# Performance work log

Hardware: AMD Instinct MI355X
Metric: run time of the kernel (lower is better)

## Reference

```python
import jax, jax.numpy as jnp
import numpy as np

B, N, DIM, H = 8, 4096, 768, 12
HD = DIM // H
SCALE = HD ** -0.5


def setup_inputs() -> dict:
    key = jax.random.key(0)
    ks = jax.random.split(key, 6)
    x = jax.random.normal(ks[0], (B, N, DIM), dtype=jnp.float32)
    # torch nn.Linear weights: [out_features, in_features]
    Wqkv = jax.random.normal(ks[1], (3 * DIM, DIM), dtype=jnp.float32) * (DIM ** -0.5)
    Wp = jax.random.normal(ks[2], (DIM, DIM), dtype=jnp.float32) * (DIM ** -0.5)
    bp = jnp.zeros((DIM,), dtype=jnp.float32)
    w_q = jax.random.normal(ks[3], (H, HD), dtype=jnp.float32)
    w_k = jax.random.normal(ks[4], (H, HD), dtype=jnp.float32)
    return {"x": x, "Wqkv": Wqkv, "Wp": Wp, "bp": bp, "w_q": w_q, "w_k": w_k}


def reference(x, Wqkv, Wp, bp, w_q, w_k):
    b, n, c = x.shape
    qkv = x @ Wqkv.T                                   # [B,N,3C]
    # rearrange 'B N (qkv H C) -> qkv B H N C'
    qkv = qkv.reshape(b, n, 3, H, HD).transpose(2, 0, 3, 1, 4)
    q, k, v = qkv[0], qkv[1], qkv[2]                   # each [B,H,N,hd]

    alpha = jnp.einsum('bhnc,hc->bhn', q, w_q) * SCALE
    alpha = jax.nn.softmax(alpha, axis=-1)             # [B,H,N]
    global_q = jnp.einsum('bhn,bhnc->bhc', alpha, q)   # [B,H,hd]

    p = global_q[:, :, None, :] * k                    # [B,H,N,hd]
    beta = jnp.einsum('bhnc,hc->bhn', p, w_k) * SCALE
    beta = jax.nn.softmax(beta, axis=-1)
    global_k = jnp.einsum('bhn,bhnc->bhc', beta, k)    # [B,H,hd]

    u = global_k[:, :, None, :] * v                    # [B,H,N,hd]
    q_flat = q.transpose(0, 2, 1, 3).reshape(b, n, c)  # 'B H N C -> B N (H C)'
    u_flat = u.transpose(0, 2, 1, 3).reshape(b, n, c)
    return u_flat @ Wp.T + bp + q_flat
```

## Files before the change

kernel.cpp:

```cpp
#include <hip/hip_runtime.h>
#include <hip/hip_bf16.h>
#include <cstdint>
#include <cstddef>

#define B_ 8
#define N_ 4096
#define DIM_ 768
#define H_ 12
#define M_ (B_*N_)
#define SCALE_ 0.125f
#define NS2 16
#define KDIM 768
#define NKT 12
#define NITER 6
#define QKS 1536

typedef __attribute__((ext_vector_type(8))) short s8v;
typedef __attribute__((ext_vector_type(4))) float f4v;

__device__ inline float bf2f(unsigned short u) {
    unsigned v = ((unsigned)u) << 16;
    return __builtin_bit_cast(float, v);
}
__device__ inline unsigned short f2bf(float f) {
    unsigned u = __builtin_bit_cast(unsigned, f);
    return (unsigned short)((u + 0x7FFFu + ((u >> 16) & 1u)) >> 16);
}
__device__ inline void gload16(const void* g, void* l) {
    __builtin_amdgcn_global_load_lds(
        (const __attribute__((address_space(1))) void*)g,
        (__attribute__((address_space(3))) void*)l, 16, 0, 0);
}

#define BARX() __builtin_amdgcn_s_barrier()
#define PRIO1() __builtin_amdgcn_s_setprio(1)
#define PRIO0() __builtin_amdgcn_s_setprio(0)
#define VM4() asm volatile("s_waitcnt vmcnt(4)" ::: "memory")
#define VM0() asm volatile("s_waitcnt vmcnt(0)" ::: "memory")

template<int EPI>
__global__ __launch_bounds__(512, 2)
void gemm8(const unsigned short* __restrict__ A, int ldaE,
           const unsigned short* __restrict__ Bmat,
           unsigned short* __restrict__ Cb,
           const float* __restrict__ w_q,
           float* __restrict__ pv1, float* __restrict__ pms1,
           int Nc, int ntn)
{
    __shared__ __align__(16) char smem[131072];
    const int tid = threadIdx.x;
    const int l = tid & 63, w = tid >> 6;
    const int lr = l & 15, g = l >> 4;
    const int wm = w >> 2, wn = w & 3;

    const int nwg = gridDim.x, cpx = nwg >> 3;
    const int bid = blockIdx.x;
    int lg = (bid & 7) * cpx + (bid >> 3);

    size_t batch_off = 0;
    if (EPI == 2) {
        const int bb = lg / 9;
        lg -= bb * 9;
        batch_off = (size_t)bb * (DIM_ * DIM_);
    }
    const int tm = lg / ntn, tn = lg % ntn;
    const int m0 = tm * 256, n0 = tn * 256;

    const long ldaB = (long)ldaE * 2;
    const long ldbB = (long)KDIM * 2;

    const int srA = w * 8 + (l >> 3);
    const int kbs = (l & 7) * 16;
    const int kbx = kbs ^ ((srA & 7) << 4);
    long offA[2], offB[2];
    offA[0] = (long)(srA) * ldaB + kbx;
    offA[1] = (long)(128 + srA) * ldaB + kbx;
    offB[0] = (long)(((srA >> 5)) * 64 + (srA & 31)) * ldbB + kbx;
    offB[1] = (long)((2 + (srA >> 5)) * 64 + (srA & 31)) * ldbB + kbx;

    const char* Abase = (const char*)(A + batch_off + (size_t)m0 * ldaE);
    const char* Bbase = (const char*)(Bmat + (size_t)n0 * KDIM);

    const int aoff = (wm * 64 + lr) * 128;
    const int boff = (wn * 32 + lr) * 128;
    const int kx0 = (g * 16) ^ ((lr & 7) << 4);
    const int kx1 = (64 + g * 16) ^ ((lr & 7) << 4);

    f4v acc[8][4] = {};
    s8v af[4][2];
    s8v bfr[2][2][2];

#define STG_A(buf_, qm_, kt_) { \
    const char* s0_ = Abase + (long)(kt_) * 2 + (long)(qm_) * 64 * ldaB; \
    char* d0_ = smem + ((buf_) * 4 + (qm_)) * 16384 + w * 1024; \
    gload16(s0_ + offA[0], d0_); \
    gload16(s0_ + offA[1], d0_ + 8192); }

#define STG_B(buf_, qn_, kt_) { \
    const char* s0_ = Bbase + (long)(kt_) * 2 + (long)(qn_) * 32 * ldbB; \
    char* d0_ = smem + ((buf_) * 4 + 2 + (qn_)) * 16384 + w * 1024; \
    gload16(s0_ + offB[0], d0_); \
    gload16(s0_ + offB[1], d0_ + 8192); }

#define DS_A(buf_, qm_) { \
    const char* ba_ = smem + ((buf_) * 4 + (qm_)) * 16384 + aoff; \
    af[0][0] = *(const s8v*)(ba_ +    0 + kx0); af[0][1] = *(const s8v*)(ba_ +    0 + kx1); \
    af[1][0] = *(const s8v*)(ba_ + 2048 + kx0); af[1][1] = *(const s8v*)(ba_ + 2048 + kx1); \
    af[2][0] = *(const s8v*)(ba_ + 4096 + kx0); af[2][1] = *(const s8v*)(ba_ + 4096 + kx1); \
    af[3][0] = *(const s8v*)(ba_ + 6144 + kx0); af[3][1] = *(const s8v*)(ba_ + 6144 + kx1); }

#define DS_B(buf_, qn_) { \
    const char* bb_ = smem + ((buf_) * 4 + 2 + (qn_)) * 16384 + boff; \
    bfr[qn_][0][0] = *(const s8v*)(bb_ +    0 + kx0); bfr[qn_][0][1] = *(const s8v*)(bb_ +    0 + kx1); \
    bfr[qn_][1][0] = *(const s8v*)(bb_ + 2048 + kx0); bfr[qn_][1][1] = *(const s8v*)(bb_ + 2048 + kx1); }

#define MM(fmg_, fng_, qn_, kk_) \
    acc[fmg_][fng_] = __builtin_amdgcn_mfma_f32_16x16x32_bf16(af[(fmg_)&3][kk_], bfr[qn_][(fng_)&1][kk_], acc[fmg_][fng_], 0, 0, 0);

#define MFMA8(qm_, qn_, kk_) \
    MM((qm_)*4+0, (qn_)*2+0, qn_, kk_) MM((qm_)*4+0, (qn_)*2+1, qn_, kk_) \
    MM((qm_)*4+1, (qn_)*2+0, qn_, kk_) MM((qm_)*4+1, (qn_)*2+1, qn_, kk_) \
    MM((qm_)*4+2, (qn_)*2+0, qn_, kk_) MM((qm_)*4+2, (qn_)*2+1, qn_, kk_) \
    MM((qm_)*4+3, (qn_)*2+0, qn_, kk_) MM((qm_)*4+3, (qn_)*2+1, qn_, kk_)

#define MFMA16(qm_, qn_) { MFMA8(qm_, qn_, 0) MFMA8(qm_, qn_, 1) }

    STG_A(0, 0, 0); STG_B(0, 0, 0); STG_A(0, 1, 0); STG_B(0, 1, 0);
    STG_A(1, 0, 64); STG_B(1, 0, 64);
    VM4(); BARX();

    for (int i = 0; i < NITER; ++i) {
        const int t1k = (2 * i + 1) * 64, t2k = (2 * i + 2) * 64, t3k = (2 * i + 3) * 64;
        const bool h2 = (2 * i + 2) < NKT, h3 = (2 * i + 3) < NKT;
        const bool last = (i == NITER - 1);
        DS_A(0, 0); DS_B(0, 0); STG_B(1, 1, t1k);
        BARX(); PRIO1(); MFMA16(0, 0); PRIO0(); BARX();
        DS_B(0, 1); STG_A(1, 1, t1k);
        BARX(); PRIO1(); MFMA16(0, 1); PRIO0(); BARX();
        DS_A(0, 1); if (h2) STG_A(0, 0, t2k);
        BARX(); PRIO1(); MFMA16(1, 0); PRIO0(); BARX();
        if (h2) STG_B(0, 0, t2k);
        BARX(); PRIO1(); MFMA16(1, 1); PRIO0();
        if (last) { VM0(); } else { VM4(); }
        BARX();
        DS_A(1, 0); DS_B(1, 0); if (h2) STG_A(0, 1, t2k);
        BARX(); PRIO1(); MFMA16(0, 0); PRIO0(); BARX();
        DS_B(1, 1); if (h2) STG_B(0, 1, t2k);
        BARX(); PRIO1(); MFMA16(0, 1); PRIO0(); BARX();
        DS_A(1, 1); if (h3) STG_A(1, 0, t3k);
        BARX(); PRIO1(); MFMA16(1, 0); PRIO0(); BARX();
        if (h3) STG_B(1, 0, t3k);
        BARX(); PRIO1(); MFMA16(1, 1); PRIO0();
        if (last) { VM0(); } else { VM4(); }
        BARX();
    }

#pragma unroll
    for (int fmg = 0; fmg < 8; ++fmg) {
#pragma unroll
        for (int fng = 0; fng < 4; ++fng) {
            const int col = n0 + wn * 64 + fng * 16 + lr;
#pragma unroll
            for (int r = 0; r < 4; ++r) {
                const int row = m0 + wm * 128 + fmg * 16 + g * 4 + r;
                Cb[batch_off + (size_t)row * Nc + col] = f2bf(acc[fmg][fng][r]);
            }
        }
    }

    if (EPI == 0 && tn < 3) {
        const int h = tn * 4 + wn;
        float wq[4];
#pragma unroll
        for (int f = 0; f < 4; ++f) wq[f] = w_q[h * 64 + f * 16 + lr];

        float d[8][4];
#pragma unroll
        for (int fmg = 0; fmg < 8; ++fmg) {
#pragma unroll
            for (int r = 0; r < 4; ++r) {
                float s = acc[fmg][0][r] * wq[0] + acc[fmg][1][r] * wq[1]
                        + acc[fmg][2][r] * wq[2] + acc[fmg][3][r] * wq[3];
                s += __shfl_xor(s, 1); s += __shfl_xor(s, 2);
                s += __shfl_xor(s, 4); s += __shfl_xor(s, 8);
                d[fmg][r] = s * SCALE_;
            }
        }
        float mw = d[0][0];
#pragma unroll
        for (int fmg = 0; fmg < 8; ++fmg)
#pragma unroll
            for (int r = 0; r < 4; ++r) mw = fmaxf(mw, d[fmg][r]);
        mw = fmaxf(mw, __shfl_xor(mw, 16));
        mw = fmaxf(mw, __shfl_xor(mw, 32));

        float ssum = 0.f;
        float pvec[4] = {};
#pragma unroll
        for (int fmg = 0; fmg < 8; ++fmg) {
#pragma unroll
            for (int r = 0; r < 4; ++r) {
                const float e = __expf(d[fmg][r] - mw);
                ssum += e;
#pragma unroll
                for (int f = 0; f < 4; ++f) pvec[f] += e * acc[fmg][f][r];
            }
        }
        ssum += __shfl_xor(ssum, 16); ssum += __shfl_xor(ssum, 32);
#pragma unroll
        for (int f = 0; f < 4; ++f) {
            pvec[f] += __shfl_xor(pvec[f], 16);
            pvec[f] += __shfl_xor(pvec[f], 32);
        }

        const int b = m0 >> 12;
        const int bh = b * H_ + h;
        const int slice = ((m0 & (N_ - 1)) >> 7) + wm;
        if (g == 0) {
#pragma unroll
            for (int f = 0; f < 4; ++f)
                pv1[(size_t)(bh * 32 + slice) * 64 + f * 16 + lr] = pvec[f];
            if (lr == 0) {
                pms1[(bh * 32 + slice) * 2] = mw;
                pms1[(bh * 32 + slice) * 2 + 1] = ssum;
            }
        }
    }
#undef STG_A
#undef STG_B
#undef DS_A
#undef DS_B
#undef MM
#undef MFMA8
#undef MFMA16
}

__global__ __launch_bounds__(512, 2)
void gemm128(const unsigned short* __restrict__ A, int ldaE,
             const unsigned short* __restrict__ Bmat,
             float* __restrict__ Cf,
             const float* __restrict__ bias, const unsigned short* __restrict__ Qf,
             int Nc, int ntn)
{
    __shared__ __align__(16) char smem[98304];
    const int tid = threadIdx.x;
    const int l = tid & 63, w = tid >> 6;
    const int lr = l & 15, g = l >> 4;
    const int wm = w >> 2, wn = w & 3;

    const int nwg = gridDim.x, cpx = nwg >> 3;
    const int bid = blockIdx.x;
    const int lg = (bid & 7) * cpx + (bid >> 3);
    const int tm = lg / ntn, tn = lg % ntn;
    const int m0 = tm * 128, n0 = tn * 256;

    const long ldaB = (long)ldaE * 2;
    const long ldbB = (long)KDIM * 2;

    const unsigned short* Bp = Bmat + (size_t)(m0 >> 12) * (DIM_ * DIM_);

    const int srA = w * 8 + (l >> 3);
    const int kbs = (l & 7) * 16;
    const int kbx = kbs ^ ((srA & 7) << 4);
    long offA[2], offB[2];
    offA[0] = (long)(srA) * ldaB + kbx;
    offA[1] = (long)(64 + srA) * ldaB + kbx;
    offB[0] = (long)(((srA >> 5)) * 64 + (srA & 31)) * ldbB + kbx;
    offB[1] = (long)((2 + (srA >> 5)) * 64 + (srA & 31)) * ldbB + kbx;

    const char* Abase = (const char*)(A + (size_t)m0 * ldaE);
    const char* Bbase = (const char*)(Bp + (size_t)n0 * KDIM);

    const int aoff = (wm * 64 + lr) * 128;
    const int boff = (wn * 32 + lr) * 128;
    const int kx0 = (g * 16) ^ ((lr & 7) << 4);
    const int kx1 = (64 + g * 16) ^ ((lr & 7) << 4);

    f4v acc[4][4] = {};
    s8v af[4][2];
    s8v bfr[2][2][2];

#define STG_A1(buf_, kt_) { \
    const char* s0_ = Abase + (long)(kt_) * 2; \
    char* d0_ = smem + ((buf_) * 3) * 16384 + w * 1024; \
    gload16(s0_ + offA[0], d0_); \
    gload16(s0_ + offA[1], d0_ + 8192); }

#define STG_B1(buf_, qn_, kt_) { \
    const char* s0_ = Bbase + (long)(kt_) * 2 + (long)(qn_) * 32 * ldbB; \
    char* d0_ = smem + ((buf_) * 3 + 1 + (qn_)) * 16384 + w * 1024; \
    gload16(s0_ + offB[0], d0_); \
    gload16(s0_ + offB[1], d0_ + 8192); }

#define DS_A1(buf_) { \
    const char* ba_ = smem + ((buf_) * 3) * 16384 + aoff; \
    af[0][0] = *(const s8v*)(ba_ +    0 + kx0); af[0][1] = *(const s8v*)(ba_ +    0 + kx1); \
    af[1][0] = *(const s8v*)(ba_ + 2048 + kx0); af[1][1] = *(const s8v*)(ba_ + 2048 + kx1); \
    af[2][0] = *(const s8v*)(ba_ + 4096 + kx0); af[2][1] = *(const s8v*)(ba_ + 4096 + kx1); \
    af[3][0] = *(const s8v*)(ba_ + 6144 + kx0); af[3][1] = *(const s8v*)(ba_ + 6144 + kx1); }

#define DS_B1(buf_, qn_) { \
    const char* bb_ = smem + ((buf_) * 3 + 1 + (qn_)) * 16384 + boff; \
    bfr[qn_][0][0] = *(const s8v*)(bb_ +    0 + kx0); bfr[qn_][0][1] = *(const s8v*)(bb_ +    0 + kx1); \
    bfr[qn_][1][0] = *(const s8v*)(bb_ + 2048 + kx0); bfr[qn_][1][1] = *(const s8v*)(bb_ + 2048 + kx1); }

#define MM1(fm_, fng_, qn_, kk_) \
    acc[fm_][fng_] = __builtin_amdgcn_mfma_f32_16x16x32_bf16(af[fm_][kk_], bfr[qn_][(fng_)&1][kk_], acc[fm_][fng_], 0, 0, 0);

#define MFMA16_1(qn_, kk_) \
    MM1(0, (qn_)*2+0, qn_, kk_) MM1(0, (qn_)*2+1, qn_, kk_) \
    MM1(1, (qn_)*2+0, qn_, kk_) MM1(1, (qn_)*2+1, qn_, kk_) \
    MM1(2, (qn_)*2+0, qn_, kk_) MM1(2, (qn_)*2+1, qn_, kk_) \
    MM1(3, (qn_)*2+0, qn_, kk_) MM1(3, (qn_)*2+1, qn_, kk_)

#define MFMA32_1(qn_) { MFMA16_1(qn_, 0) MFMA16_1(qn_, 1) }

    STG_A1(0, 0); STG_B1(0, 0, 0); STG_B1(0, 1, 0);
    STG_A1(1, 64); STG_B1(1, 0, 64);
    VM4(); BARX();

    for (int i = 0; i < NITER; ++i) {
        const int t1k = (2 * i + 1) * 64, t2k = (2 * i + 2) * 64, t3k = (2 * i + 3) * 64;
        const bool h2 = (2 * i + 2) < NKT, h3 = (2 * i + 3) < NKT;
        const bool last = (i == NITER - 1);
        DS_A1(0); DS_B1(0, 0); STG_B1(1, 1, t1k);
        BARX(); PRIO1(); MFMA32_1(0); PRIO0(); BARX();
        DS_B1(0, 1); if (h2) { STG_A1(0, t2k); STG_B1(0, 0, t2k); }
        BARX(); PRIO1(); MFMA32_1(1); PRIO0();
        if (last) { VM0(); } else { VM4(); }
        BARX();
        DS_A1(1); DS_B1(1, 0); if (h2) STG_B1(0, 1, t2k);
        BARX(); PRIO1(); MFMA32_1(0); PRIO0(); BARX();
        DS_B1(1, 1); if (h3) { STG_A1(1, t3k); STG_B1(1, 0, t3k); }
        BARX(); PRIO1(); MFMA32_1(1); PRIO0();
        if (last) { VM0(); } else { VM4(); }
        BARX();
    }

#pragma unroll
    for (int fm = 0; fm < 4; ++fm) {
#pragma unroll
        for (int fng = 0; fng < 4; ++fng) {
            const int col = n0 + wn * 64 + fng * 16 + lr;
#pragma unroll
            for (int r = 0; r < 4; ++r) {
                const int row = m0 + wm * 64 + fm * 16 + g * 4 + r;
                Cf[(size_t)row * Nc + col] = acc[fm][fng][r] + bias[col]
                                             + bf2f(Qf[(size_t)row * QKS + col]);
            }
        }
    }
#undef STG_A1
#undef STG_B1
#undef DS_A1
#undef DS_B1
#undef MM1
#undef MFMA16_1
#undef MFMA32_1
}

__global__ __launch_bounds__(256)
void fused_path(const unsigned short* __restrict__ qkv, int col_off,
                const float* __restrict__ vec, int per_bh,
                float* __restrict__ partv, float* __restrict__ partms)
{
    const int bid = blockIdx.x;
    const int bh = bid / NS2, sp = bid % NS2;
    const int b = bh / H_, h = bh % H_;
    const int t = threadIdx.x;
    const int lane8 = t & 7, grp = t >> 3;

    const unsigned short* base = qkv + ((size_t)(b * N_ + sp * 256) * QKS)
                                 + col_off + h * 64 + lane8 * 8;
    const float* wv = vec + (per_bh ? bh * 64 : h * 64) + lane8 * 8;
    float w8[8];
#pragma unroll
    for (int j = 0; j < 8; j++) w8[j] = wv[j];

    float q[8][8];
    float d[8];
#pragma unroll
    for (int pass = 0; pass < 8; ++pass) {
        const int row = pass * 32 + grp;
        s8v q8 = *(const s8v*)(base + (size_t)row * QKS);
        float s = 0.f;
#pragma unroll
        for (int j = 0; j < 8; j++) {
            q[pass][j] = bf2f((unsigned short)q8[j]);
            s += q[pass][j] * w8[j];
        }
        s += __shfl_xor(s, 1); s += __shfl_xor(s, 2); s += __shfl_xor(s, 4);
        d[pass] = s * SCALE_;
    }
    float m = d[0];
#pragma unroll
    for (int pass = 1; pass < 8; ++pass) m = fmaxf(m, d[pass]);
    float ssum = 0.f;
    float a8[8] = {};
#pragma unroll
    for (int pass = 0; pass < 8; ++pass) {
        float e = __expf(d[pass] - m);
        ssum += e;
#pragma unroll
        for (int j = 0; j < 8; j++) a8[j] += e * q[pass][j];
    }

    __shared__ float Lm[32], Ls[32];
    __shared__ float La[32][64];
    if (lane8 == 0) { Lm[grp] = m; Ls[grp] = ssum; }
#pragma unroll
    for (int j = 0; j < 8; j++) La[grp][lane8 * 8 + j] = a8[j];
    __syncthreads();

    if (t < 64) {
        float mstar = Lm[0];
#pragma unroll
        for (int g2 = 1; g2 < 32; ++g2) mstar = fmaxf(mstar, Lm[g2]);
        float sstar = 0.f, v = 0.f;
#pragma unroll
        for (int g2 = 0; g2 < 32; ++g2) {
            float e = __expf(Lm[g2] - mstar);
            sstar += Ls[g2] * e;
            v += La[g2][t] * e;
        }
        partv[(size_t)bid * 64 + t] = v;
        if (t == 0) { partms[bid * 2] = mstar; partms[bid * 2 + 1] = sstar; }
    }
}

__global__ void path_reduce(const float* __restrict__ partv, const float* __restrict__ partms,
                            int nsp, float* __restrict__ gout,
                            const float* __restrict__ wk, float* __restrict__ bvec)
{
    const int bh = blockIdx.x;
    const int t = threadIdx.x;
    const int h = bh % H_;
    float mstar = partms[(bh * nsp) * 2];
    for (int p = 1; p < nsp; ++p) mstar = fmaxf(mstar, partms[(bh * nsp + p) * 2]);
    float sstar = 0.f, v = 0.f;
    for (int p = 0; p < nsp; ++p) {
        float e = __expf(partms[(bh * nsp + p) * 2] - mstar);
        sstar += partms[(bh * nsp + p) * 2 + 1] * e;
        v += partv[(size_t)(bh * nsp + p) * 64 + t] * e;
    }
    float g = v / sstar;
    gout[bh * 64 + t] = g;
    if (wk) bvec[bh * 64 + t] = g * wk[h * 64 + t];
}

__global__ void cvt_all(const float* __restrict__ x, const float* __restrict__ Wqkv,
                        unsigned short* __restrict__ xb, unsigned short* __restrict__ wqkb,
                        unsigned short* __restrict__ wvT,
                        int n4x, int n4xw)
{
    int i = blockIdx.x * 256 + threadIdx.x;
    if (i < n4xw) {
        const float* src; unsigned short* dst; int k;
        if (i < n4x) { src = x; dst = xb; k = i; }
        else { src = Wqkv; dst = wqkb; k = i - n4x; }
        float4 v = ((const float4*)src)[k];
        ushort4 o;
        o.x = f2bf(v.x); o.y = f2bf(v.y); o.z = f2bf(v.z); o.w = f2bf(v.w);
        ((ushort4*)dst)[k] = o;
    } else {
        const int k = i - n4xw;
        const int ii = k % DIM_;
        const int c0 = (k / DIM_) * 4;
        ushort4 o;
        o.x = f2bf(Wqkv[(size_t)(2 * DIM_ + c0 + 0) * DIM_ + ii]);
        o.y = f2bf(Wqkv[(size_t)(2 * DIM_ + c0 + 1) * DIM_ + ii]);
        o.z = f2bf(Wqkv[(size_t)(2 * DIM_ + c0 + 2) * DIM_ + ii]);
        o.w = f2bf(Wqkv[(size_t)(2 * DIM_ + c0 + 3) * DIM_ + ii]);
        *(ushort4*)&wvT[(size_t)ii * DIM_ + c0] = o;
    }
}

__global__ __launch_bounds__(256)
void fold_wp(const float* __restrict__ Wp, const float* __restrict__ gk,
             unsigned short* __restrict__ W2)
{
    int idx = blockIdx.x * 256 + threadIdx.x;
    int e4 = idx * 4;
    int b = (int)((unsigned)e4 / (unsigned)(DIM_ * DIM_));
    int rem = e4 - b * (DIM_ * DIM_);
    int c = rem % DIM_;
    float4 wv = *(const float4*)&Wp[rem];
    const float* gp = &gk[b * DIM_ + c];
    ushort4 o;
    o.x = f2bf(wv.x * gp[0]); o.y = f2bf(wv.y * gp[1]);
    o.z = f2bf(wv.z * gp[2]); o.w = f2bf(wv.w * gp[3]);
    *(ushort4*)&W2[e4] = o;
}

extern "C" void kernel_launch(void* const* d_in, const int* in_sizes, int n_in,
                              void* d_out, int out_size, void* d_ws, size_t ws_size,
                              hipStream_t stream)
{
    const float* x    = (const float*)d_in[0];
    const float* Wqkv = (const float*)d_in[1];
    const float* Wp   = (const float*)d_in[2];
    const float* bp   = (const float*)d_in[3];
    const float* w_q  = (const float*)d_in[4];
    const float* w_k  = (const float*)d_in[5];
    float* out = (float*)d_out;

    constexpr size_t NXB  = (size_t)M_ * DIM_;
    constexpr size_t NWQK = (size_t)2 * DIM_ * DIM_;
    constexpr size_t NWV  = (size_t)DIM_ * DIM_;
    constexpr size_t NQK  = (size_t)M_ * QKS;
    constexpr size_t NW2  = (size_t)B_ * DIM_ * DIM_;

    char* p = (char*)d_ws;
    unsigned short* xb    = (unsigned short*)p; p += NXB * 2;
    unsigned short* wqkb  = (unsigned short*)p; p += NWQK * 2;
    unsigned short* wvT   = (unsigned short*)p; p += NWV * 2;
    unsigned short* qkb   = (unsigned short*)p; p += NQK * 2;
    unsigned short* w2b   = (unsigned short*)p; p += NW2 * 2;
    unsigned short* w3b   = (unsigned short*)p; p += NW2 * 2;
    float* pv1  = (float*)p; p += (size_t)B_ * H_ * 32 * 64 * 4;
    float* pms1 = (float*)p; p += (size_t)B_ * H_ * 32 * 2 * 4;
    float* pv2  = (float*)p; p += (size_t)B_ * H_ * NS2 * 64 * 4;
    float* pms2 = (float*)p; p += (size_t)B_ * H_ * NS2 * 2 * 4;
    float* gq   = (float*)p; p += (size_t)B_ * H_ * 64 * 4;
    float* bvec = (float*)p; p += (size_t)B_ * H_ * 64 * 4;
    float* gkv  = (float*)p; p += (size_t)B_ * H_ * 64 * 4;

    constexpr int N4X  = (int)(NXB / 4);
    constexpr int N4XW = N4X + (int)(NWQK / 4);
    constexpr int NTOT = N4XW + (int)(NWV / 4);
    cvt_all<<<NTOT / 256, 256, 0, stream>>>(x, Wqkv, xb, wqkb, wvT, N4X, N4XW);

    gemm8<0><<<128 * 6, 512, 0, stream>>>(xb, DIM_, wqkb, qkb, w_q, pv1, pms1, QKS, 6);

    path_reduce<<<B_ * H_, 64, 0, stream>>>(pv1, pms1, 32, gq, w_k, bvec);

    fused_path<<<B_ * H_ * NS2, 256, 0, stream>>>(qkb, DIM_, bvec, 1, pv2, pms2);
    path_reduce<<<B_ * H_, 64, 0, stream>>>(pv2, pms2, NS2, gkv, nullptr, nullptr);

    fold_wp<<<(int)(NW2 / 4 / 256), 256, 0, stream>>>(Wp, gkv, w2b);

    gemm8<2><<<72, 512, 0, stream>>>(w2b, DIM_, wvT, w3b, nullptr, nullptr, nullptr,
                                     DIM_, 3);

    gemm128<<<256 * 3, 512, 0, stream>>>(xb, DIM_, w3b, out, bp, qkb, DIM_, 3);
}
```

Baseline: 236.9 us.

## Fold q residual into projection weights and fuse first path reduction

The q residual is folded algebraically into the per-batch combined weight: gemm8<2> now adds the fp32 Wq rows to the folded Wp*diag(gk)*Wv product, so the final GEMM no longer reads q from a workspace. Because of this, the QKV GEMM stops storing q entirely and writes only the k columns into a narrower buffer. The first path_reduce is merged into the k-path kernel, and each block recomputes global_q from the partials, which removes one launch. The cost is redundant per-block reduction work and q entering the final GEMM at bf16 precision through the weights, with its rounding behaviour changed.

```diff
diff --git a/kernel.cpp b/kernel.cpp
--- a/kernel.cpp
+++ b/kernel.cpp
@@ -13,7 +13,6 @@
 #define KDIM 768
 #define NKT 12
 #define NITER 6
-#define QKS 1536
 
 typedef __attribute__((ext_vector_type(8))) short s8v;
 typedef __attribute__((ext_vector_type(4))) float f4v;
@@ -45,7 +44,8 @@
            unsigned short* __restrict__ Cb,
            const float* __restrict__ w_q,
            float* __restrict__ pv1, float* __restrict__ pms1,
-           int Nc, int ntn)
+           const float* __restrict__ addW,
+           int ntn)
 {
     __shared__ __align__(16) char smem[131072];
     const int tid = threadIdx.x;
@@ -155,15 +155,34 @@
         BARX();
     }
 
-#pragma unroll
-    for (int fmg = 0; fmg < 8; ++fmg) {
-#pragma unroll
-        for (int fng = 0; fng < 4; ++fng) {
-            const int col = n0 + wn * 64 + fng * 16 + lr;
-#pragma unroll
-            for (int r = 0; r < 4; ++r) {
-                const int row = m0 + wm * 128 + fmg * 16 + g * 4 + r;
-                Cb[batch_off + (size_t)row * Nc + col] = f2bf(acc[fmg][fng][r]);
+    if (EPI == 0) {
+        if (tn >= 3) {
+            const int c0 = (tn - 3) * 256;
+#pragma unroll
+            for (int fmg = 0; fmg < 8; ++fmg) {
+#pragma unroll
+                for (int fng = 0; fng < 4; ++fng) {
+                    const int col = c0 + wn * 64 + fng * 16 + lr;
+#pragma unroll
+                    for (int r = 0; r < 4; ++r) {
+                        const int row = m0 + wm * 128 + fmg * 16 + g * 4 + r;
+                        Cb[(size_t)row * DIM_ + col] = f2bf(acc[fmg][fng][r]);
+                    }
+                }
+            }
+        }
+    } else {
+#pragma unroll
+        for (int fmg = 0; fmg < 8; ++fmg) {
+#pragma unroll
+            for (int fng = 0; fng < 4; ++fng) {
+                const int col = n0 + wn * 64 + fng * 16 + lr;
+#pragma unroll
+                for (int r = 0; r < 4; ++r) {
+                    const int row = m0 + wm * 128 + fmg * 16 + g * 4 + r;
+                    Cb[batch_off + (size_t)row * DIM_ + col] =
+                        f2bf(acc[fmg][fng][r] + addW[(size_t)row * DIM_ + col]);
+                }
             }
         }
     }
@@ -239,7 +258,7 @@
 void gemm128(const unsigned short* __restrict__ A, int ldaE,
              const unsigned short* __restrict__ Bmat,
              float* __restrict__ Cf,
-             const float* __restrict__ bias, const unsigned short* __restrict__ Qf,
+             const float* __restrict__ bias,
              int Nc, int ntn)
 {
     __shared__ __align__(16) char smem[98304];
@@ -345,8 +364,7 @@
 #pragma unroll
             for (int r = 0; r < 4; ++r) {
                 const int row = m0 + wm * 64 + fm * 16 + g * 4 + r;
-                Cf[(size_t)row * Nc + col] = acc[fm][fng][r] + bias[col]
-                                             + bf2f(Qf[(size_t)row * QKS + col]);
+                Cf[(size_t)row * Nc + col] = acc[fm][fng][r] + bias[col];
             }
         }
     }
@@ -360,9 +378,10 @@
 }
 
 __global__ __launch_bounds__(256)
-void fused_path(const unsigned short* __restrict__ qkv, int col_off,
-                const float* __restrict__ vec, int per_bh,
-                float* __restrict__ partv, float* __restrict__ partms)
+void fused_b(const unsigned short* __restrict__ kb,
+             const float* __restrict__ pv1, const float* __restrict__ pms1,
+             const float* __restrict__ w_k,
+             float* __restrict__ pv2, float* __restrict__ pms2)
 {
     const int bid = blockIdx.x;
     const int bh = bid / NS2, sp = bid % NS2;
@@ -370,19 +389,34 @@
     const int t = threadIdx.x;
     const int lane8 = t & 7, grp = t >> 3;
 
-    const unsigned short* base = qkv + ((size_t)(b * N_ + sp * 256) * QKS)
-                                 + col_off + h * 64 + lane8 * 8;
-    const float* wv = vec + (per_bh ? bh * 64 : h * 64) + lane8 * 8;
+    __shared__ float gq_s[64];
+    if (t < 64) {
+        float mstar = pms1[(bh * 32) * 2];
+#pragma unroll
+        for (int p = 1; p < 32; ++p) mstar = fmaxf(mstar, pms1[(bh * 32 + p) * 2]);
+        float sstar = 0.f, v = 0.f;
+#pragma unroll
+        for (int p = 0; p < 32; ++p) {
+            const float e = __expf(pms1[(bh * 32 + p) * 2] - mstar);
+            sstar += pms1[(bh * 32 + p) * 2 + 1] * e;
+            v += pv1[(size_t)(bh * 32 + p) * 64 + t] * e;
+        }
+        gq_s[t] = (v / sstar) * w_k[h * 64 + t];
+    }
+    __syncthreads();
+
     float w8[8];
 #pragma unroll
-    for (int j = 0; j < 8; j++) w8[j] = wv[j];
-
+    for (int j = 0; j < 8; j++) w8[j] = gq_s[lane8 * 8 + j];
+
+    const unsigned short* base = kb + ((size_t)(b * N_ + sp * 256) * DIM_)
+                                 + h * 64 + lane8 * 8;
     float q[8][8];
     float d[8];
 #pragma unroll
     for (int pass = 0; pass < 8; ++pass) {
         const int row = pass * 32 + grp;
-        s8v q8 = *(const s8v*)(base + (size_t)row * QKS);
+        s8v q8 = *(const s8v*)(base + (size_t)row * DIM_);
         float s = 0.f;
 #pragma unroll
         for (int j = 0; j < 8; j++) {
@@ -423,18 +457,16 @@
             sstar += Ls[g2] * e;
             v += La[g2][t] * e;
         }
-        partv[(size_t)bid * 64 + t] = v;
-        if (t == 0) { partms[bid * 2] = mstar; partms[bid * 2 + 1] = sstar; }
+        pv2[(size_t)bid * 64 + t] = v;
+        if (t == 0) { pms2[bid * 2] = mstar; pms2[bid * 2 + 1] = sstar; }
     }
 }
 
 __global__ void path_reduce(const float* __restrict__ partv, const float* __restrict__ partms,
-                            int nsp, float* __restrict__ gout,
-                            const float* __restrict__ wk, float* __restrict__ bvec)
+                            int nsp, float* __restrict__ gout)
 {
     const int bh = blockIdx.x;
     const int t = threadIdx.x;
-    const int h = bh % H_;
     float mstar = partms[(bh * nsp) * 2];
     for (int p = 1; p < nsp; ++p) mstar = fmaxf(mstar, partms[(bh * nsp + p) * 2]);
     float sstar = 0.f, v = 0.f;
@@ -443,9 +475,7 @@
         sstar += partms[(bh * nsp + p) * 2 + 1] * e;
         v += partv[(size_t)(bh * nsp + p) * 64 + t] * e;
     }
-    float g = v / sstar;
-    gout[bh * 64 + t] = g;
-    if (wk) bvec[bh * 64 + t] = g * wk[h * 64 + t];
+    gout[bh * 64 + t] = v / sstar;
 }
 
 __global__ void cvt_all(const float* __restrict__ x, const float* __restrict__ Wqkv,
@@ -507,22 +537,20 @@
     constexpr size_t NXB  = (size_t)M_ * DIM_;
     constexpr size_t NWQK = (size_t)2 * DIM_ * DIM_;
     constexpr size_t NWV  = (size_t)DIM_ * DIM_;
-    constexpr size_t NQK  = (size_t)M_ * QKS;
+    constexpr size_t NKB  = (size_t)M_ * DIM_;
     constexpr size_t NW2  = (size_t)B_ * DIM_ * DIM_;
 
     char* p = (char*)d_ws;
     unsigned short* xb    = (unsigned short*)p; p += NXB * 2;
     unsigned short* wqkb  = (unsigned short*)p; p += NWQK * 2;
     unsigned short* wvT   = (unsigned short*)p; p += NWV * 2;
-    unsigned short* qkb   = (unsigned short*)p; p += NQK * 2;
+    unsigned short* kb    = (unsigned short*)p; p += NKB * 2;
     unsigned short* w2b   = (unsigned short*)p; p += NW2 * 2;
-    unsigned short* w3b   = (unsigned short*)p; p += NW2 * 2;
+    unsigned short* w4b   = (unsigned short*)p; p += NW2 * 2;
     float* pv1  = (float*)p; p += (size_t)B_ * H_ * 32 * 64 * 4;
     float* pms1 = (float*)p; p += (size_t)B_ * H_ * 32 * 2 * 4;
     float* pv2  = (float*)p; p += (size_t)B_ * H_ * NS2 * 64 * 4;
     float* pms2 = (float*)p; p += (size_t)B_ * H_ * NS2 * 2 * 4;
-    float* gq   = (float*)p; p += (size_t)B_ * H_ * 64 * 4;
-    float* bvec = (float*)p; p += (size_t)B_ * H_ * 64 * 4;
     float* gkv  = (float*)p; p += (size_t)B_ * H_ * 64 * 4;
 
     constexpr int N4X  = (int)(NXB / 4);
@@ -530,17 +558,17 @@
     constexpr int NTOT = N4XW + (int)(NWV / 4);
     cvt_all<<<NTOT / 256, 256, 0, stream>>>(x, Wqkv, xb, wqkb, wvT, N4X, N4XW);
 
-    gemm8<0><<<128 * 6, 512, 0, stream>>>(xb, DIM_, wqkb, qkb, w_q, pv1, pms1, QKS, 6);
-
-    path_reduce<<<B_ * H_, 64, 0, stream>>>(pv1, pms1, 32, gq, w_k, bvec);
-
-    fused_path<<<B_ * H_ * NS2, 256, 0, stream>>>(qkb, DIM_, bvec, 1, pv2, pms2);
-    path_reduce<<<B_ * H_, 64, 0, stream>>>(pv2, pms2, NS2, gkv, nullptr, nullptr);
+    gemm8<0><<<128 * 6, 512, 0, stream>>>(xb, DIM_, wqkb, kb, w_q, pv1, pms1,
+                                          nullptr, 6);
+
+    fused_b<<<B_ * H_ * NS2, 256, 0, stream>>>(kb, pv1, pms1, w_k, pv2, pms2);
+
+    path_reduce<<<B_ * H_, 64, 0, stream>>>(pv2, pms2, NS2, gkv);
 
     fold_wp<<<(int)(NW2 / 4 / 256), 256, 0, stream>>>(Wp, gkv, w2b);
 
-    gemm8<2><<<72, 512, 0, stream>>>(w2b, DIM_, wvT, w3b, nullptr, nullptr, nullptr,
-                                     DIM_, 3);
-
-    gemm128<<<256 * 3, 512, 0, stream>>>(xb, DIM_, w3b, out, bp, qkb, DIM_, 3);
-}
+    gemm8<2><<<72, 512, 0, stream>>>(w2b, DIM_, wvT, w4b, nullptr, nullptr, nullptr,
+                                     Wqkv, 3);
+
+    gemm128<<<256 * 3, 512, 0, stream>>>(xb, DIM_, w4b, out, bp, DIM_, 3);
+}
```

New measurement: 217.4 us. 1.09x faster.
